# Kernel tuning notes

Hardware: AMD Instinct MI355X
Metric: run time of the kernel (lower is better)

The kernel has to match this reference:

```python
import jax, jax.numpy as jnp
import numpy as np

B, S, D = 2, 2048, 2048
H, HKV, HD = 16, 4, 128
GROUPS = H // HKV
SCALE = HD ** -0.5
ROPE_THETA = 10000.0
NEG = -1e9


def _rope_cos_sin():
    inv_freq = 1.0 / (ROPE_THETA ** (jnp.arange(0, HD, 2, dtype=jnp.float32) / HD))  # [HD/2]
    pos = jnp.arange(S, dtype=jnp.float32)
    freqs = pos[:, None] * inv_freq[None, :]            # [S, HD/2]
    emb = jnp.concatenate([freqs, freqs], axis=-1)      # [S, HD]
    cos = jnp.broadcast_to(jnp.cos(emb)[None], (B, S, HD))
    sin = jnp.broadcast_to(jnp.sin(emb)[None], (B, S, HD))
    return cos, sin


def setup_inputs() -> dict:
    key = jax.random.key(0)
    ks = jax.random.split(key, 5)
    hidden_states = jax.random.normal(ks[0], (B, S, D), dtype=jnp.float32)
    cos, sin = _rope_cos_sin()
    causal = jnp.where(jnp.arange(S)[:, None] >= jnp.arange(S)[None, :], 0.0, NEG).astype(jnp.float32)
    attn_mask = jnp.broadcast_to(causal[None, None], (B, 1, S, S))
    wq = jax.random.normal(ks[1], (H * HD, D), dtype=jnp.float32) * (D ** -0.5)
    wk = jax.random.normal(ks[2], (HKV * HD, D), dtype=jnp.float32) * (D ** -0.5)
    wv = jax.random.normal(ks[3], (HKV * HD, D), dtype=jnp.float32) * (D ** -0.5)
    wo = jax.random.normal(ks[4], (D, H * HD), dtype=jnp.float32) * (D ** -0.5)
    return {"hidden_states": hidden_states, "cos": cos, "sin": sin,
            "attn_mask": attn_mask, "wq": wq, "wk": wk, "wv": wv, "wo": wo}


def _rotate_half(x):
    x1, x2 = x[..., : HD // 2], x[..., HD // 2:]
    return jnp.concatenate([-x2, x1], axis=-1)


def reference(hidden_states, cos, sin, attn_mask, wq, wk, wv, wo):
    # projections (torch Linear: x @ W.T), reshape to [B, heads, S, HD]
    q = (hidden_states @ wq.T).reshape(B, S, H, HD).transpose(0, 2, 1, 3)
    k = (hidden_states @ wk.T).reshape(B, S, HKV, HD).transpose(0, 2, 1, 3)
    v = (hidden_states @ wv.T).reshape(B, S, HKV, HD).transpose(0, 2, 1, 3)
    # RoPE (cos/sin broadcast over head dim)
    c = cos[:, None, :, :]
    s = sin[:, None, :, :]
    q = q * c + _rotate_half(q) * s
    k = k * c + _rotate_half(k) * s
    # GQA: repeat each kv head GROUPS times consecutively (matches repeat_kv)
    k = jnp.repeat(k, GROUPS, axis=1)
    v = jnp.repeat(v, GROUPS, axis=1)
    logits = jnp.einsum('bhqd,bhkd->bhqk', q, k) * SCALE + attn_mask
    w = jax.nn.softmax(logits.astype(jnp.float32), axis=-1).astype(q.dtype)
    out = jnp.einsum('bhqk,bhkd->bhqd', w, v)            # [B,H,S,HD]
    out = out.transpose(0, 2, 1, 3).reshape(B, S, H * HD)
    return out @ wo.T
```

## Files before the change

### kernel.cpp

```cpp
#include <hip/hip_runtime.h>

typedef __attribute__((ext_vector_type(8))) short bf16x8;
typedef __attribute__((ext_vector_type(4))) float f32x4;
typedef __attribute__((ext_vector_type(16))) float f32x16;
typedef __attribute__((ext_vector_type(8))) unsigned short u16x8;
typedef __attribute__((ext_vector_type(4))) unsigned u32x4;
typedef unsigned short u16;

#define GLOBAL_AS __attribute__((address_space(1)))
#define LDS_AS __attribute__((address_space(3)))

#define S_ 2048
#define SMK_ 0.12751741406106783f

static __device__ __forceinline__ u16 f2bf(float f) {
  unsigned u = __builtin_bit_cast(unsigned, f);
  u += 0x7fffu + ((u >> 16) & 1u);
  return (u16)(u >> 16);
}
static __device__ __forceinline__ float bf2f(u16 h) {
  return __builtin_bit_cast(float, ((unsigned)h) << 16);
}
static __device__ __forceinline__ float exp2_raw(float x) {
  float r; asm("v_exp_f32 %0, %1" : "=v"(r) : "v"(x)); return r;
}
static __device__ __forceinline__ unsigned cvtpk(float lo, float hi_) {
  unsigned r; asm("v_cvt_pk_bf16_f32 %0, %1, %2" : "=v"(r) : "v"(lo), "v"(hi_)); return r;
}

__global__ __launch_bounds__(256)
void cvt_all(const float* __restrict__ h, const float* __restrict__ wq,
             const float* __restrict__ wk, const float* __restrict__ wv,
             const float* __restrict__ wo, u16* __restrict__ Xbf,
             u16* __restrict__ Wqkv, u16* __restrict__ Wo) {
  const int bid = blockIdx.x;
  const float* src; u16* dst; long base;
  if (bid < 4096)      { src = h;  dst = Xbf;            base = (long)bid * 2048; }
  else if (bid < 6144) { src = wq; dst = Wqkv;           base = (long)(bid - 4096) * 2048; }
  else if (bid < 6656) { src = wk; dst = Wqkv + 4194304; base = (long)(bid - 6144) * 2048; }
  else if (bid < 7168) { src = wv; dst = Wqkv + 5242880; base = (long)(bid - 6656) * 2048; }
  else                 { src = wo; dst = Wo;             base = (long)(bid - 7168) * 2048; }
  const long i = base + (long)threadIdx.x * 8;
  f32x4 a = *(const f32x4*)(src + i);
  f32x4 b = *(const f32x4*)(src + i + 4);
  u16x8 o;
  o[0] = f2bf(a[0]); o[1] = f2bf(a[1]); o[2] = f2bf(a[2]); o[3] = f2bf(a[3]);
  o[4] = f2bf(b[0]); o[5] = f2bf(b[1]); o[6] = f2bf(b[2]); o[7] = f2bf(b[3]);
  *(u16x8*)(dst + i) = o;
}

template <int NJ, bool BF16OUT>
__global__ __launch_bounds__(512, 2)
void gemm256(const u16* __restrict__ A, const u16* __restrict__ Bw,
             void* __restrict__ Cp, int M, int N, int K) {
  __shared__ u16 LA[4][2][4096];
  __shared__ u16 LB[4][NJ / 2][4096];

  const int tid = threadIdx.x;
  const int wave = tid >> 6, lane = tid & 63;
  const int fr = lane & 15, fg = lane >> 4;
  const int wm = (wave >> 2) * 128;
  const int wn = (wave & 3) * (NJ * 16);
  const long rowA = (long)blockIdx.y * 256;
  const long rowB = (long)blockIdx.x * (NJ * 64);

  const int srow = tid >> 2;
  const int sc8 = (tid & 3) ^ (srow & 3);
  const int wbase = wave * 512;

  const int nt = K >> 5;

  f32x4 acc[8][NJ] = {};

#define STAGE_A(pt)                                                          \
  {                                                                          \
    const int _b = (pt) & 3;                                                 \
    const long _k = (long)(pt) * 32 + sc8 * 8;                               \
    __builtin_amdgcn_global_load_lds(                                        \
        (GLOBAL_AS void*)(A + (rowA + srow) * K + _k),                       \
        (LDS_AS void*)(&LA[_b][0][wbase]), 16, 0, 0);                        \
    __builtin_amdgcn_global_load_lds(                                        \
        (GLOBAL_AS void*)(A + (rowA + 128 + srow) * K + _k),                 \
        (LDS_AS void*)(&LA[_b][1][wbase]), 16, 0, 0);                        \
  }
#define STAGE_B(pt)                                                          \
  {                                                                          \
    const int _b = (pt) & 3;                                                 \
    const long _k = (long)(pt) * 32 + sc8 * 8;                               \
    __builtin_amdgcn_global_load_lds(                                        \
        (GLOBAL_AS void*)(Bw + (rowB + srow) * K + _k),                      \
        (LDS_AS void*)(&LB[_b][0][wbase]), 16, 0, 0);                        \
    if (NJ == 4)                                                             \
      __builtin_amdgcn_global_load_lds(                                      \
          (GLOBAL_AS void*)(Bw + (rowB + 128 + srow) * K + _k),              \
          (LDS_AS void*)(&LB[_b][NJ / 2 - 1][wbase]), 16, 0, 0);             \
  }

  STAGE_A(0); STAGE_B(0);
  STAGE_A(1); STAGE_B(1);
  STAGE_A(2); STAGE_B(2);

  for (int t = 0; t < nt; ++t) {
    const int rem = nt - 1 - t;
    if (NJ == 4) {
      if (rem >= 2)      asm volatile("s_waitcnt vmcnt(8)" ::: "memory");
      else if (rem == 1) asm volatile("s_waitcnt vmcnt(4)" ::: "memory");
      else               asm volatile("s_waitcnt vmcnt(0)" ::: "memory");
    } else {
      if (rem >= 2)      asm volatile("s_waitcnt vmcnt(6)" ::: "memory");
      else if (rem == 1) asm volatile("s_waitcnt vmcnt(3)" ::: "memory");
      else               asm volatile("s_waitcnt vmcnt(0)" ::: "memory");
    }
    __builtin_amdgcn_s_barrier();

    const u16* Ah = LA[t & 3][wm >> 7];
    const u16* Bh = LB[t & 3][NJ == 4 ? (wn >> 7) : 0];
    const bool pf = (t + 3) < nt;

    bf16x8 af0[4], bfv[NJ];
#pragma unroll
    for (int mi = 0; mi < 4; ++mi) {
      const int rl = mi * 16 + fr;
      af0[mi] = *(const bf16x8*)&Ah[rl * 32 + ((fg ^ (rl & 3)) << 3)];
    }
#pragma unroll
    for (int nj = 0; nj < NJ; ++nj) {
      const int rb = (wn & 127) + nj * 16 + fr;
      bfv[nj] = *(const bf16x8*)&Bh[rb * 32 + ((fg ^ (rb & 3)) << 3)];
    }
    if (pf) STAGE_A(t + 3);
    __builtin_amdgcn_s_setprio(1);
#pragma unroll
    for (int mi = 0; mi < 4; ++mi)
#pragma unroll
      for (int nj = 0; nj < NJ; ++nj)
        acc[mi][nj] = __builtin_amdgcn_mfma_f32_16x16x32_bf16(af0[mi], bfv[nj], acc[mi][nj], 0, 0, 0);
    __builtin_amdgcn_s_setprio(0);

    bf16x8 af1[4];
#pragma unroll
    for (int mi = 0; mi < 4; ++mi) {
      const int rl = 64 + mi * 16 + fr;
      af1[mi] = *(const bf16x8*)&Ah[rl * 32 + ((fg ^ (rl & 3)) << 3)];
    }
    if (pf) STAGE_B(t + 3);
    __builtin_amdgcn_s_setprio(1);
#pragma unroll
    for (int mi = 0; mi < 4; ++mi)
#pragma unroll
      for (int nj = 0; nj < NJ; ++nj)
        acc[4 + mi][nj] = __builtin_amdgcn_mfma_f32_16x16x32_bf16(af1[mi], bfv[nj], acc[4 + mi][nj], 0, 0, 0);
    __builtin_amdgcn_s_setprio(0);

    __builtin_amdgcn_s_barrier();
  }
#undef STAGE_A
#undef STAGE_B

#pragma unroll
  for (int mi = 0; mi < 8; ++mi)
#pragma unroll
    for (int nj = 0; nj < NJ; ++nj)
#pragma unroll
      for (int r = 0; r < 4; ++r) {
        const long row = rowA + wm + mi * 16 + fg * 4 + r;
        const long col = rowB + wn + nj * 16 + fr;
        if (BF16OUT) ((u16*)Cp)[row * N + col] = f2bf(acc[mi][nj][r]);
        else         ((float*)Cp)[row * N + col] = acc[mi][nj][r];
      }
}

__global__ __launch_bounds__(256)
void rope_rearrange(const u16* __restrict__ QKV, const float* __restrict__ cosb,
                    const float* __restrict__ sinb, u16* __restrict__ Qr,
                    u16* __restrict__ Kr) {
  const int m = blockIdx.x;
  const int b = m >> 11, s = m & 2047;
  const int t = threadIdx.x;
  const u16* row = QKV + (long)m * 3072;
  const float* cp = cosb + (long)m * 128;
  const float* sp = sinb + (long)m * 128;
#pragma unroll
  for (int i = 0; i < 4; ++i) {
    const int idx = i * 256 + t;
    const int h = idx >> 6, d = idx & 63;
    const float x1 = bf2f(row[h * 128 + d]);
    const float x2 = bf2f(row[h * 128 + d + 64]);
    const float c = cp[d], sv = sp[d];
    const long o = ((long)(b * 16 + h) * S_ + s) * 128 + d;
    Qr[o] = f2bf(x1 * c - x2 * sv);
    Qr[o + 64] = f2bf(x2 * c + x1 * sv);
  }
  {
    const int h = t >> 6, d = t & 63;
    const float x1 = bf2f(row[2048 + h * 128 + d]);
    const float x2 = bf2f(row[2048 + h * 128 + d + 64]);
    const float c = cp[d], sv = sp[d];
    const long o = ((long)(b * 4 + h) * S_ + s) * 128 + d;
    Kr[o] = f2bf((x1 * c - x2 * sv) * SMK_);
    Kr[o + 64] = f2bf((x2 * c + x1 * sv) * SMK_);
  }
}

__global__ __launch_bounds__(256)
void transpose_v(const u16* __restrict__ QKV, u16* __restrict__ Vt) {
  __shared__ u16 t[32][33];
  const int s0 = blockIdx.x * 32, d0 = blockIdx.y * 32;
  const int bk = blockIdx.z;
  const int b = bk >> 2, kh = bk & 3;
  const int tx = threadIdx.x & 31, ty = threadIdx.x >> 5;
  const u16* src = QKV + 2560 + (long)kh * 128;
#pragma unroll
  for (int i = 0; i < 4; ++i) {
    const int sl = ty + i * 8;
    t[sl][tx] = src[(long)(b * S_ + s0 + sl) * 3072 + d0 + tx];
  }
  __syncthreads();
  u16* dst = Vt + (long)(b * 4 + kh) * 128 * S_;
#pragma unroll
  for (int i = 0; i < 4; ++i) {
    const int dl = ty + i * 8;
    dst[(long)(d0 + dl) * S_ + s0 + tx] = t[tx][dl];
  }
}

struct PA2 { bf16x8 a, b; };
static __device__ __forceinline__ PA2 pack_half(const f32x16 s) {
  PA2 out;
#pragma unroll
  for (int ks2 = 0; ks2 < 2; ++ks2) {
    const int rb = ks2 * 8;
    unsigned w0 = cvtpk(s[rb + 0], s[rb + 1]);
    unsigned w1 = cvtpk(s[rb + 2], s[rb + 3]);
    unsigned w2 = cvtpk(s[rb + 4], s[rb + 5]);
    unsigned w3 = cvtpk(s[rb + 6], s[rb + 7]);
    asm("v_permlane32_swap_b32 %0, %1" : "+v"(w0), "+v"(w2));
    asm("v_permlane32_swap_b32 %0, %1" : "+v"(w1), "+v"(w3));
    u32x4 pw; pw[0] = w0; pw[1] = w1; pw[2] = w2; pw[3] = w3;
    if (ks2 == 0) out.a = __builtin_bit_cast(bf16x8, pw);
    else          out.b = __builtin_bit_cast(bf16x8, pw);
  }
  return out;
}

template <int NH>
static __device__ __forceinline__ void attn_tile(
    const u16* __restrict__ Ks, const u16* __restrict__ Vs,
    const bf16x8 (&qf)[8], f32x16 (&acc)[4], float& m_run, float& l_run,
    const int kv0, const int qwmin, const int qg, const int l31,
    const int hi, const int r7) {
  f32x16 s[NH];
#pragma unroll
  for (int hh = 0; hh < NH; ++hh) s[hh] = (f32x16){};
  __builtin_amdgcn_s_setprio(1);
#pragma unroll
  for (int ds = 0; ds < 8; ++ds) {
    const int ch = ((2 * ds + hi) ^ r7) << 3;
#pragma unroll
    for (int hh = 0; hh < NH; ++hh) {
      const bf16x8 ka = *(const bf16x8*)&Ks[(hh * 32 + l31) * 128 + ch];
      s[hh] = __builtin_amdgcn_mfma_f32_32x32x16_bf16(ka, qf[ds], s[hh], 0, 0, 0);
    }
  }
  __builtin_amdgcn_s_setprio(0);

  if (kv0 + NH * 32 - 1 > qwmin) {
#pragma unroll
    for (int hh = 0; hh < NH; ++hh)
#pragma unroll
      for (int r = 0; r < 16; ++r) {
        const int cr = (r & 3) + 8 * (r >> 2) + 4 * hi;
        if (kv0 + hh * 32 + cr > qg) s[hh][r] = -3.0e38f;
      }
  }

  float mx = s[0][0];
#pragma unroll
  for (int hh = 0; hh < NH; ++hh)
#pragma unroll
    for (int r = 0; r < 16; ++r) mx = fmaxf(mx, s[hh][r]);
  mx = fmaxf(mx, __shfl_xor(mx, 32));

  if (__any(mx > m_run + 8.0f)) {
    const float mn = fmaxf(m_run, mx);
    const float scq = exp2_raw(m_run - mn);
    m_run = mn; l_run *= scq;
#pragma unroll
    for (int r = 0; r < 16; ++r) {
      const int cr = (r & 3) + 8 * (r >> 2) + 4 * hi;
      const float sr = __shfl(scq, cr);
      acc[0][r] *= sr; acc[1][r] *= sr; acc[2][r] *= sr; acc[3][r] *= sr;
    }
  }

  float rs = 0.f;
#pragma unroll
  for (int hh = 0; hh < NH; ++hh)
#pragma unroll
    for (int r = 0; r < 16; ++r) { s[hh][r] = exp2_raw(s[hh][r] - m_run); rs += s[hh][r]; }
  rs += __shfl_xor(rs, 32);
  l_run += rs;

  bf16x8 pa[2 * NH];
#pragma unroll
  for (int hh = 0; hh < NH; ++hh) {
    const PA2 p = pack_half(s[hh]);
    pa[2 * hh] = p.a; pa[2 * hh + 1] = p.b;
  }
  __builtin_amdgcn_s_setprio(1);
#pragma unroll
  for (int nj = 0; nj < 4; ++nj) {
    const int vrow = (nj * 32 + l31) * 64;
#pragma unroll
    for (int ks = 0; ks < 2 * NH; ++ks) {
      const bf16x8 vf = *(const bf16x8*)&Vs[vrow + (((2 * ks + hi) ^ r7) << 3)];
      acc[nj] = __builtin_amdgcn_mfma_f32_32x32x16_bf16(pa[ks], vf, acc[nj], 0, 0, 0);
    }
  }
  __builtin_amdgcn_s_setprio(0);
}

#define NUNITS 1024
__global__ __launch_bounds__(128)
void attn_fwd(const u16* __restrict__ Qr, const u16* __restrict__ Kr,
              const u16* __restrict__ Vt, u16* __restrict__ Att,
              unsigned* __restrict__ ctr) {
  __shared__ u16 Ks[64 * 128];
  __shared__ u16 Vs[128 * 64];
  __shared__ unsigned s_uid;

  const int tid = threadIdx.x, wave = tid >> 6, lane = tid & 63;
  const int l31 = lane & 31, hi = lane >> 5, r7 = lane & 7;

  for (;;) {
    __syncthreads();
    if (tid == 0) s_uid = atomicAdd(ctr, 1u);
    __syncthreads();
    const unsigned uid = s_uid;
    if (uid >= NUNITS) break;

    const int qt = 31 - (int)(uid >> 5);
    const int bh = uid & 31;
    const int b = bh >> 4, h = bh & 15;
    const int kh = h >> 2;
    const int qwmin = qt * 64 + wave * 32;

    const u16* Qb = Qr + (long)(b * 16 + h) * S_ * 128;
    const u16* Kb = Kr + (long)(b * 4 + kh) * S_ * 128;
    const u16* Vg = Vt + (long)(b * 4 + kh) * 128 * (long)S_;

    bf16x8 qf[8];
    const u16* qrow = Qb + (long)(qwmin + l31) * 128 + hi * 8;
#pragma unroll
    for (int ds = 0; ds < 8; ++ds) qf[ds] = *(const bf16x8*)(qrow + ds * 16);

    f32x16 acc[4] = {};
    float m_run = -1e30f, l_run = 0.f;
    const int qg = qwmin + l31;

    const int ntiles = qt + 1;
    for (int t = 0; t < ntiles; ++t) {
      const int kv0 = t * 64;
      __syncthreads();
#pragma unroll
      for (int c = 0; c < 8; ++c) {
        const int slab = wave * 8 + c;
        const int offu = slab * 512 + lane * 8;
        const int kvl = offu >> 7;
        const int kc = ((offu >> 3) & 15) ^ (kvl & 7);
        __builtin_amdgcn_global_load_lds(
            (GLOBAL_AS void*)(Kb + (long)(kv0 + kvl) * 128 + kc * 8),
            (LDS_AS void*)(Ks + slab * 512), 16, 0, 0);
        const int dr = offu >> 6;
        const int vc = ((offu >> 3) & 7) ^ (dr & 7);
        __builtin_amdgcn_global_load_lds(
            (GLOBAL_AS void*)(Vg + (long)dr * S_ + kv0 + vc * 8),
            (LDS_AS void*)(Vs + slab * 512), 16, 0, 0);
      }
      __syncthreads();

      if (kv0 + 32 <= qwmin + 31)
        attn_tile<2>(Ks, Vs, qf, acc, m_run, l_run, kv0, qwmin, qg, l31, hi, r7);
      else if (kv0 <= qwmin + 31)
        attn_tile<1>(Ks, Vs, qf, acc, m_run, l_run, kv0, qwmin, qg, l31, hi, r7);
    }

    const float inv = 1.0f / l_run;
#pragma unroll
    for (int r = 0; r < 16; ++r) {
      const int cr = (r & 3) + 8 * (r >> 2) + 4 * hi;
      const float ir = __shfl(inv, cr);
      const long orow = ((long)b * S_ + qt * 64 + wave * 32 + cr) * 2048 + h * 128 + l31;
      Att[orow]      = f2bf(acc[0][r] * ir);
      Att[orow + 32] = f2bf(acc[1][r] * ir);
      Att[orow + 64] = f2bf(acc[2][r] * ir);
      Att[orow + 96] = f2bf(acc[3][r] * ir);
    }
  }
}

extern "C" void kernel_launch(void* const* d_in, const int* in_sizes, int n_in,
                              void* d_out, int out_size, void* d_ws, size_t ws_size,
                              hipStream_t stream) {
  const float* hidden = (const float*)d_in[0];
  const float* cosb = (const float*)d_in[1];
  const float* sinb = (const float*)d_in[2];
  const float* wq = (const float*)d_in[4];
  const float* wk = (const float*)d_in[5];
  const float* wv = (const float*)d_in[6];
  const float* wo = (const float*)d_in[7];
  float* out = (float*)d_out;

  u16* Xbf  = (u16*)d_ws;
  u16* Wqkv = Xbf + 8388608;
  u16* Wo   = Wqkv + 6291456;
  u16* QKV  = Wo + 4194304;
  u16* Qr   = QKV + 12582912;
  u16* Kr   = Qr + 8388608;
  u16* Vtp  = Kr + 2097152;
  u16* Att  = Xbf;
  if (ws_size < (size_t)44040192 * 2) return;

  cvt_all<<<dim3(9216), dim3(256), 0, stream>>>(hidden, wq, wk, wv, wo, Xbf, Wqkv, Wo);
  gemm256<4, true><<<dim3(12, 16), dim3(512), 0, stream>>>(Xbf, Wqkv, (void*)QKV, 4096, 3072, 2048);
  rope_rearrange<<<dim3(4096), dim3(256), 0, stream>>>(QKV, cosb, sinb, Qr, Kr);
  transpose_v<<<dim3(64, 4, 8), dim3(256), 0, stream>>>(QKV, Vtp);
  hipMemsetAsync((void*)Wqkv, 0, 4, stream);
  attn_fwd<<<dim3(768), dim3(128), 0, stream>>>(Qr, Kr, Vtp, Att, (unsigned*)Wqkv);
  gemm256<2, false><<<dim3(16, 16), dim3(512), 0, stream>>>(Att, Wo, (void*)out, 4096, 2048, 2048);
}
```

Measured before the change: 224.6 us.

## Split K and V staging to prefetch next tile during attention compute

The attention loop now issues K loads for the next tile right after QK^T finishes, and V loads for the next tile after PV finishes. Each load is guarded by targeted vmcnt waits and raw barriers instead of full __syncthreads. This overlaps global-to-LDS transfer with softmax and MFMA work rather than stalling at the top of each tile. The templated tile helper is also inlined with a per-wave diagonal flag that skips the upper half-block. The hand-counted vmcnt values are fragile and must match the exact number of outstanding loads.

```diff
diff --git a/kernel.cpp b/kernel.cpp
--- a/kernel.cpp
+++ b/kernel.cpp
@@ -243,83 +243,6 @@
   return out;
 }
 
-template <int NH>
-static __device__ __forceinline__ void attn_tile(
-    const u16* __restrict__ Ks, const u16* __restrict__ Vs,
-    const bf16x8 (&qf)[8], f32x16 (&acc)[4], float& m_run, float& l_run,
-    const int kv0, const int qwmin, const int qg, const int l31,
-    const int hi, const int r7) {
-  f32x16 s[NH];
-#pragma unroll
-  for (int hh = 0; hh < NH; ++hh) s[hh] = (f32x16){};
-  __builtin_amdgcn_s_setprio(1);
-#pragma unroll
-  for (int ds = 0; ds < 8; ++ds) {
-    const int ch = ((2 * ds + hi) ^ r7) << 3;
-#pragma unroll
-    for (int hh = 0; hh < NH; ++hh) {
-      const bf16x8 ka = *(const bf16x8*)&Ks[(hh * 32 + l31) * 128 + ch];
-      s[hh] = __builtin_amdgcn_mfma_f32_32x32x16_bf16(ka, qf[ds], s[hh], 0, 0, 0);
-    }
-  }
-  __builtin_amdgcn_s_setprio(0);
-
-  if (kv0 + NH * 32 - 1 > qwmin) {
-#pragma unroll
-    for (int hh = 0; hh < NH; ++hh)
-#pragma unroll
-      for (int r = 0; r < 16; ++r) {
-        const int cr = (r & 3) + 8 * (r >> 2) + 4 * hi;
-        if (kv0 + hh * 32 + cr > qg) s[hh][r] = -3.0e38f;
-      }
-  }
-
-  float mx = s[0][0];
-#pragma unroll
-  for (int hh = 0; hh < NH; ++hh)
-#pragma unroll
-    for (int r = 0; r < 16; ++r) mx = fmaxf(mx, s[hh][r]);
-  mx = fmaxf(mx, __shfl_xor(mx, 32));
-
-  if (__any(mx > m_run + 8.0f)) {
-    const float mn = fmaxf(m_run, mx);
-    const float scq = exp2_raw(m_run - mn);
-    m_run = mn; l_run *= scq;
-#pragma unroll
-    for (int r = 0; r < 16; ++r) {
-      const int cr = (r & 3) + 8 * (r >> 2) + 4 * hi;
-      const float sr = __shfl(scq, cr);
-      acc[0][r] *= sr; acc[1][r] *= sr; acc[2][r] *= sr; acc[3][r] *= sr;
-    }
-  }
-
-  float rs = 0.f;
-#pragma unroll
-  for (int hh = 0; hh < NH; ++hh)
-#pragma unroll
-    for (int r = 0; r < 16; ++r) { s[hh][r] = exp2_raw(s[hh][r] - m_run); rs += s[hh][r]; }
-  rs += __shfl_xor(rs, 32);
-  l_run += rs;
-
-  bf16x8 pa[2 * NH];
-#pragma unroll
-  for (int hh = 0; hh < NH; ++hh) {
-    const PA2 p = pack_half(s[hh]);
-    pa[2 * hh] = p.a; pa[2 * hh + 1] = p.b;
-  }
-  __builtin_amdgcn_s_setprio(1);
-#pragma unroll
-  for (int nj = 0; nj < 4; ++nj) {
-    const int vrow = (nj * 32 + l31) * 64;
-#pragma unroll
-    for (int ks = 0; ks < 2 * NH; ++ks) {
-      const bf16x8 vf = *(const bf16x8*)&Vs[vrow + (((2 * ks + hi) ^ r7) << 3)];
-      acc[nj] = __builtin_amdgcn_mfma_f32_32x32x16_bf16(pa[ks], vf, acc[nj], 0, 0, 0);
-    }
-  }
-  __builtin_amdgcn_s_setprio(0);
-}
-
 #define NUNITS 1024
 __global__ __launch_bounds__(128)
 void attn_fwd(const u16* __restrict__ Qr, const u16* __restrict__ Kr,
@@ -332,6 +255,31 @@
   const int tid = threadIdx.x, wave = tid >> 6, lane = tid & 63;
   const int l31 = lane & 31, hi = lane >> 5, r7 = lane & 7;
 
+#define STAGE_K(tt)                                                           \
+  {                                                                           \
+    _Pragma("unroll") for (int c = 0; c < 8; ++c) {                           \
+      const int slab = wave * 8 + c;                                          \
+      const int offu = slab * 512 + lane * 8;                                 \
+      const int kvl = offu >> 7;                                              \
+      const int kc = ((offu >> 3) & 15) ^ (kvl & 7);                          \
+      __builtin_amdgcn_global_load_lds(                                       \
+          (GLOBAL_AS void*)(Kb + (long)((tt) * 64 + kvl) * 128 + kc * 8),     \
+          (LDS_AS void*)(Ks + slab * 512), 16, 0, 0);                         \
+    }                                                                         \
+  }
+#define STAGE_V(tt)                                                           \
+  {                                                                           \
+    _Pragma("unroll") for (int c = 0; c < 8; ++c) {                           \
+      const int slab = wave * 8 + c;                                          \
+      const int offu = slab * 512 + lane * 8;                                 \
+      const int dr = offu >> 6;                                               \
+      const int vc = ((offu >> 3) & 7) ^ (dr & 7);                            \
+      __builtin_amdgcn_global_load_lds(                                       \
+          (GLOBAL_AS void*)(Vg + (long)dr * S_ + (tt) * 64 + vc * 8),         \
+          (LDS_AS void*)(Vs + slab * 512), 16, 0, 0);                         \
+    }                                                                         \
+  }
+
   for (;;) {
     __syncthreads();
     if (tid == 0) s_uid = atomicAdd(ctr, 1u);
@@ -358,31 +306,109 @@
     float m_run = -1e30f, l_run = 0.f;
     const int qg = qwmin + l31;
 
+    STAGE_K(0);
+    STAGE_V(0);
+
     const int ntiles = qt + 1;
     for (int t = 0; t < ntiles; ++t) {
       const int kv0 = t * 64;
-      __syncthreads();
-#pragma unroll
-      for (int c = 0; c < 8; ++c) {
-        const int slab = wave * 8 + c;
-        const int offu = slab * 512 + lane * 8;
-        const int kvl = offu >> 7;
-        const int kc = ((offu >> 3) & 15) ^ (kvl & 7);
-        __builtin_amdgcn_global_load_lds(
-            (GLOBAL_AS void*)(Kb + (long)(kv0 + kvl) * 128 + kc * 8),
-            (LDS_AS void*)(Ks + slab * 512), 16, 0, 0);
-        const int dr = offu >> 6;
-        const int vc = ((offu >> 3) & 7) ^ (dr & 7);
-        __builtin_amdgcn_global_load_lds(
-            (GLOBAL_AS void*)(Vg + (long)dr * S_ + kv0 + vc * 8),
-            (LDS_AS void*)(Vs + slab * 512), 16, 0, 0);
-      }
-      __syncthreads();
-
-      if (kv0 + 32 <= qwmin + 31)
-        attn_tile<2>(Ks, Vs, qf, acc, m_run, l_run, kv0, qwmin, qg, l31, hi, r7);
-      else if (kv0 <= qwmin + 31)
-        attn_tile<1>(Ks, Vs, qf, acc, m_run, l_run, kv0, qwmin, qg, l31, hi, r7);
+      const bool more = (t + 1) < ntiles;
+      const bool fullw = !(t == qt && wave == 0);
+
+      asm volatile("s_waitcnt vmcnt(8)" ::: "memory");
+      __builtin_amdgcn_s_barrier();
+
+      f32x16 s0 = {}, s1 = {};
+      __builtin_amdgcn_s_setprio(1);
+#pragma unroll
+      for (int ds = 0; ds < 8; ++ds) {
+        const int ch = ((2 * ds + hi) ^ r7) << 3;
+        const bf16x8 ka0 = *(const bf16x8*)&Ks[l31 * 128 + ch];
+        s0 = __builtin_amdgcn_mfma_f32_32x32x16_bf16(ka0, qf[ds], s0, 0, 0, 0);
+      }
+      if (fullw) {
+#pragma unroll
+        for (int ds = 0; ds < 8; ++ds) {
+          const int ch = ((2 * ds + hi) ^ r7) << 3;
+          const bf16x8 ka1 = *(const bf16x8*)&Ks[(32 + l31) * 128 + ch];
+          s1 = __builtin_amdgcn_mfma_f32_32x32x16_bf16(ka1, qf[ds], s1, 0, 0, 0);
+        }
+      }
+      __builtin_amdgcn_s_setprio(0);
+
+      asm volatile("s_waitcnt lgkmcnt(0)" ::: "memory");
+      __builtin_amdgcn_s_barrier();
+      if (more) STAGE_K(t + 1);
+
+      if (t == qt) {
+#pragma unroll
+        for (int r = 0; r < 16; ++r) {
+          const int cr = (r & 3) + 8 * (r >> 2) + 4 * hi;
+          if (kv0 + cr > qg) s0[r] = -3.0e38f;
+          if (fullw && kv0 + 32 + cr > qg) s1[r] = -3.0e38f;
+        }
+      }
+
+      float mx = s0[0];
+#pragma unroll
+      for (int r = 1; r < 16; ++r) mx = fmaxf(mx, s0[r]);
+      if (fullw) {
+#pragma unroll
+        for (int r = 0; r < 16; ++r) mx = fmaxf(mx, s1[r]);
+      }
+      mx = fmaxf(mx, __shfl_xor(mx, 32));
+
+      if (__any(mx > m_run + 8.0f)) {
+        const float mn = fmaxf(m_run, mx);
+        const float scq = exp2_raw(m_run - mn);
+        m_run = mn; l_run *= scq;
+#pragma unroll
+        for (int r = 0; r < 16; ++r) {
+          const int cr = (r & 3) + 8 * (r >> 2) + 4 * hi;
+          const float sr = __shfl(scq, cr);
+          acc[0][r] *= sr; acc[1][r] *= sr; acc[2][r] *= sr; acc[3][r] *= sr;
+        }
+      }
+
+      float rs = 0.f;
+#pragma unroll
+      for (int r = 0; r < 16; ++r) { s0[r] = exp2_raw(s0[r] - m_run); rs += s0[r]; }
+      if (fullw) {
+#pragma unroll
+        for (int r = 0; r < 16; ++r) { s1[r] = exp2_raw(s1[r] - m_run); rs += s1[r]; }
+      }
+      rs += __shfl_xor(rs, 32);
+      l_run += rs;
+
+      bf16x8 pa0, pa1, pa2, pa3;
+      { const PA2 p = pack_half(s0); pa0 = p.a; pa1 = p.b; }
+      if (fullw) { const PA2 p = pack_half(s1); pa2 = p.a; pa3 = p.b; }
+      else       { pa2 = pa0; pa3 = pa1; }
+
+      if (more) asm volatile("s_waitcnt vmcnt(8)" ::: "memory");
+      else      asm volatile("s_waitcnt vmcnt(0)" ::: "memory");
+      __builtin_amdgcn_s_barrier();
+
+      __builtin_amdgcn_s_setprio(1);
+#pragma unroll
+      for (int nj = 0; nj < 4; ++nj) {
+        const int vrow = (nj * 32 + l31) * 64;
+        const bf16x8 vf0 = *(const bf16x8*)&Vs[vrow + (((0 + hi) ^ r7) << 3)];
+        const bf16x8 vf1 = *(const bf16x8*)&Vs[vrow + (((2 + hi) ^ r7) << 3)];
+        acc[nj] = __builtin_amdgcn_mfma_f32_32x32x16_bf16(pa0, vf0, acc[nj], 0, 0, 0);
+        acc[nj] = __builtin_amdgcn_mfma_f32_32x32x16_bf16(pa1, vf1, acc[nj], 0, 0, 0);
+        if (fullw) {
+          const bf16x8 vf2 = *(const bf16x8*)&Vs[vrow + (((4 + hi) ^ r7) << 3)];
+          const bf16x8 vf3 = *(const bf16x8*)&Vs[vrow + (((6 + hi) ^ r7) << 3)];
+          acc[nj] = __builtin_amdgcn_mfma_f32_32x32x16_bf16(pa2, vf2, acc[nj], 0, 0, 0);
+          acc[nj] = __builtin_amdgcn_mfma_f32_32x32x16_bf16(pa3, vf3, acc[nj], 0, 0, 0);
+        }
+      }
+      __builtin_amdgcn_s_setprio(0);
+
+      asm volatile("s_waitcnt lgkmcnt(0)" ::: "memory");
+      __builtin_amdgcn_s_barrier();
+      if (more) STAGE_V(t + 1);
     }
 
     const float inv = 1.0f / l_run;
@@ -397,6 +423,8 @@
       Att[orow + 96] = f2bf(acc[3][r] * ir);
     }
   }
+#undef STAGE_K
+#undef STAGE_V
 }
 
 extern "C" void kernel_launch(void* const* d_in, const int* in_sizes, int n_in,
```

After: 228.3 us. About the same (+1.7%).
